# Optimization experiments

Hardware: AMD Instinct MI355X
Metric: run time of the kernel (lower is better)

## Reference

```python
import jax, jax.numpy as jnp
import numpy as np

B, S, Dm, H, W, G = 2, 4096, 768, 12, 256, 16
HD = Dm // H
NEG = -10000.0


def _band_qk(q, k, w):
    # q,k: [B,S,H,D] -> banded scores [B,S,H,2w+1]; slot j = key position i-w+j
    Bq, Sq, Hq, Dq = q.shape
    nb = Sq // w
    qb = q.reshape(Bq, nb, w, Hq, Dq)
    kp = jnp.pad(k, ((0, 0), (w, w), (0, 0), (0, 0)))
    idx = (jnp.arange(nb) * w)[:, None] + jnp.arange(3 * w)[None, :]
    kb = kp[:, idx]                                    # [B,nb,3w,H,D]
    s = jnp.einsum('btxhd,btyhd->bthxy', qb, kb)       # [B,nb,H,w,3w]
    r = jnp.arange(w)[:, None]
    c = r + jnp.arange(2 * w + 1)[None, :]
    band = s[..., r, c]                                # [B,nb,H,w,2w+1]
    return band.transpose(0, 1, 3, 2, 4).reshape(Bq, Sq, Hq, 2 * w + 1)


def _band_pv(p, v, w):
    # p: [B,S,H,2w+1], v: [B,S,H,D] -> [B,S,H,D]
    Bp, Sp, Hp, _ = p.shape
    Dv = v.shape[-1]
    nb = Sp // w
    vp = jnp.pad(v, ((0, 0), (w, w), (0, 0), (0, 0)))
    idx = (jnp.arange(nb) * w)[:, None] + jnp.arange(3 * w)[None, :]
    vb = vp[:, idx]                                    # [B,nb,3w,H,D]
    pb = p.reshape(Bp, nb, w, Hp, 2 * w + 1).transpose(0, 1, 3, 2, 4)
    r = jnp.arange(w)[:, None]
    c = r + jnp.arange(2 * w + 1)[None, :]
    pband = jnp.zeros((Bp, nb, Hp, w, 3 * w), p.dtype).at[..., r, c].set(pb)
    out = jnp.einsum('bthxy,btyhd->btxhd', pband, vb)  # [B,nb,w,H,D]
    return out.reshape(Bp, Sp, Hp, Dv)


def setup_inputs() -> dict:
    key = jax.random.key(0)
    ks = jax.random.split(key, 13)
    inp = {'hidden_states': jax.random.normal(ks[0], (B, S, Dm), dtype=jnp.float32)}
    names = ['Wq', 'bq', 'Wk', 'bk', 'Wv', 'bv', 'Wqg', 'bqg', 'Wkg', 'bkg', 'Wvg', 'bvg']
    for i, n in enumerate(names):
        sh = (Dm, Dm) if n.startswith('W') else (Dm,)
        inp[n] = 0.02 * jax.random.normal(ks[i + 1], sh, dtype=jnp.float32)
    inp['n_global'] = G
    return inp


def reference(hidden_states, Wq, bq, Wk, bk, Wv, bv, Wqg, bqg, Wkg, bkg, Wvg, bvg, n_global):
    Bh, Sh, D = hidden_states.shape
    hd = D // H
    w, g = W, n_global
    scale = 1.0 / jnp.sqrt(jnp.float32(hd))
    q = ((hidden_states @ Wq + bq) * scale).reshape(Bh, Sh, H, hd)
    k = (hidden_states @ Wk + bk).reshape(Bh, Sh, H, hd)
    v = (hidden_states @ Wv + bv).reshape(Bh, Sh, H, hd)
    # banded local attention scores (mask_invalid_locations -> -inf outside seq)
    band = _band_qk(q, k, w)                           # [B,S,H,2w+1]
    i = jnp.arange(Sh)[:, None]
    j = jnp.arange(2 * w + 1)[None, :]
    kpos = i - w + j                                   # key position per window slot
    valid = (kpos >= 0) & (kpos < Sh)
    band = jnp.where(valid[None, :, None, :], band, -jnp.inf)
    # remove global keys from windowed attention (-10000 float mask)
    band = band + jnp.where(valid & (kpos < g), NEG, 0.0)[None, :, None, :]
    # global columns: every query attends to global keys (local k projection)
    sel = jnp.einsum('bihd,bghd->bihg', q, k[:, :g])
    logits = jnp.concatenate([sel, band], axis=-1)     # [B,S,H,g+2w+1]
    probs = jax.nn.softmax(logits.astype(jnp.float32), axis=-1)
    attn = jnp.einsum('bihg,bghd->bihd', probs[..., :g], v[:, :g])
    attn = attn + _band_pv(probs[..., g:], v, w)       # [B,S,H,hd]
    # global token rows: full attention with global projections
    qg = ((hidden_states[:, :g] @ Wqg + bqg) * scale).reshape(Bh, g, H, hd)
    kg = (hidden_states @ Wkg + bkg).reshape(Bh, Sh, H, hd)
    vg = (hidden_states @ Wvg + bvg).reshape(Bh, Sh, H, hd)
    gl = jnp.einsum('bghd,bshd->bhgs', qg, kg)
    gp = jax.nn.softmax(gl.astype(jnp.float32), axis=-1)
    out_g = jnp.einsum('bhgs,bshd->bghd', gp, vg)      # [B,g,H,hd]
    attn = attn.at[:, :g].set(out_g)
    return attn.reshape(Bh, Sh, D)
```

## Files before the change

kernel.cpp:

```cpp
#include <hip/hip_runtime.h>

constexpr int Bc = 2, Sc = 4096, Dmc = 768, Hc = 12, HDc = 64, Wc = 256, Gc = 16;
constexpr int NCH = 16, CHK = 256;
constexpr float LOG2E = 1.4426950408889634f;
constexpr float SCALE2q = 0.125f * LOG2E;
constexpr float NEG2c = -10000.0f * LOG2E;

typedef __attribute__((ext_vector_type(8))) short s16x8;
typedef __attribute__((ext_vector_type(4))) short s16x4;
typedef __attribute__((ext_vector_type(4))) float f32x4;
typedef __attribute__((ext_vector_type(2))) unsigned int u32x2;

#define DEVINL __device__ __forceinline__

DEVINL float b2f(short x) {
  unsigned int u = ((unsigned int)(unsigned short)x) << 16;
  return __builtin_bit_cast(float, u);
}
DEVINL short f2b(float f) {
  unsigned int u = __builtin_bit_cast(unsigned int, f);
  unsigned int r = (u + 0x7fffu + ((u >> 16) & 1u)) >> 16;
  return (short)r;
}
DEVINL void gload16(const short* g, const short* l) {
  __builtin_amdgcn_global_load_lds(
      (const __attribute__((address_space(1))) void*)g,
      (__attribute__((address_space(3))) void*)l, 16, 0, 0);
}

__global__ __launch_bounds__(256) void conv_bf16(
    const float* __restrict__ src, short* __restrict__ dst)
{
  const size_t i = ((size_t)blockIdx.x * 256 + threadIdx.x) * 8;
  f32x4 a = *(const f32x4*)(src + i);
  f32x4 c = *(const f32x4*)(src + i + 4);
  s16x8 r;
#pragma unroll
  for (int u = 0; u < 4; ++u) { r[u] = f2b(a[u]); r[4 + u] = f2b(c[u]); }
  *(s16x8*)(dst + i) = r;
}

__global__ __launch_bounds__(256) void transpose_w(
    const float* __restrict__ W0, const float* __restrict__ W1, const float* __restrict__ W2,
    short* __restrict__ T0, short* __restrict__ T1, short* __restrict__ T2)
{
  const float* W = blockIdx.z == 0 ? W0 : (blockIdx.z == 1 ? W1 : W2);
  short* T = blockIdx.z == 0 ? T0 : (blockIdx.z == 1 ? T1 : T2);
  __shared__ short t[32][33];
  const int k0 = blockIdx.x * 32, n0 = blockIdx.y * 32;
  const int a = threadIdx.x >> 3, cg = (threadIdx.x & 7) * 4;
  f32x4 v = *(const f32x4*)&W[(size_t)(k0 + a) * Dmc + n0 + cg];
#pragma unroll
  for (int u = 0; u < 4; ++u) t[a][cg + u] = f2b(v[u]);
  __syncthreads();
  s16x4 s;
#pragma unroll
  for (int u = 0; u < 4; ++u) s[u] = t[cg + u][a];
  *(s16x4*)&T[(size_t)(n0 + a) * Dmc + k0 + cg] = s;
}

__global__ __launch_bounds__(256) void gemm_fused(
    const short* __restrict__ X, const short* __restrict__ Wt,
    const float* __restrict__ b0, const float* __restrict__ b1, const float* __restrict__ b2,
    short* __restrict__ Y0, float scale0)
{
  __shared__ short lds[16384];
  char* ldsb = (char*)lds;
  const int tid = threadIdx.x, lane = tid & 63, wid = tid >> 6;
  const int gy = gridDim.y;

  const int rawd = blockIdx.x + 64 * blockIdx.y;
  const int wgid = (rawd & 7) * (gy * 8) + (rawd >> 3);
  const int mi0 = wgid / gy, ny = wgid - mi0 * gy;
  const int m0 = mi0 * 128;
  const int nch = ny / 6, ncol = (ny % 6) * 128;
  const int n0g = ny * 128;

  short* Y = Y0 + (size_t)nch * 6291456;
  const float* bias = nch == 0 ? b0 : (nch == 1 ? b1 : b2);
  const float scale = nch == 0 ? scale0 : 1.0f;

  const int lr = lane & 15, lq = lane >> 4;
  const int wm = (wid & 1) * 64, wn = (wid >> 1) * 64;

  const int l8 = lane >> 3, l7 = lane & 7;
  const int colsh = ((l7 * 16) ^ (l8 << 4)) >> 1;
  const short* Aptr[4];
  const short* Bptr[4];
#pragma unroll
  for (int i = 0; i < 4; ++i) {
    Aptr[i] = X  + (size_t)(m0  + wid * 32 + i * 8 + l8) * Dmc + colsh;
    Bptr[i] = Wt + (size_t)(n0g + wid * 32 + i * 8 + l8) * Dmc + colsh;
  }

  int arb[4][2], brb[4][2];
#pragma unroll
  for (int mi = 0; mi < 4; ++mi)
#pragma unroll
    for (int ks = 0; ks < 2; ++ks) {
      int row = wm + mi * 16 + lr;
      arb[mi][ks] = row * 128 + ((lq * 16 + ks * 64) ^ ((row & 7) << 4));
    }
#pragma unroll
  for (int ni = 0; ni < 4; ++ni)
#pragma unroll
    for (int ks = 0; ks < 2; ++ks) {
      int row = wn + ni * 16 + lr;
      brb[ni][ks] = 16384 + row * 128 + ((lq * 16 + ks * 64) ^ ((row & 7) << 4));
    }

  f32x4 acc[4][4] = {};

  for (int kt = 0; kt < 12; ++kt) {
    const int ko = kt * 64;
    if (kt) __syncthreads();
#pragma unroll
    for (int i = 0; i < 4; ++i) {
      gload16(Aptr[i] + ko, &lds[wid * 2048 + i * 512]);
      gload16(Bptr[i] + ko, &lds[8192 + wid * 2048 + i * 512]);
    }
    asm volatile("s_waitcnt vmcnt(0)" ::: "memory");
    __syncthreads();
#pragma unroll
    for (int ks = 0; ks < 2; ++ks) {
      s16x8 af[4], bf[4];
#pragma unroll
      for (int mi = 0; mi < 4; ++mi) af[mi] = *(const s16x8*)(ldsb + arb[mi][ks]);
#pragma unroll
      for (int ni = 0; ni < 4; ++ni) bf[ni] = *(const s16x8*)(ldsb + brb[ni][ks]);
#pragma unroll
      for (int mi = 0; mi < 4; ++mi)
#pragma unroll
        for (int ni = 0; ni < 4; ++ni)
          acc[mi][ni] = __builtin_amdgcn_mfma_f32_16x16x32_bf16(af[mi], bf[ni], acc[mi][ni], 0, 0, 0);
    }
  }

#pragma unroll
  for (int mi = 0; mi < 4; ++mi)
#pragma unroll
    for (int ni = 0; ni < 4; ++ni) {
      int col = ncol + wn + ni * 16 + lr;
      float bv_ = bias[col];
#pragma unroll
      for (int r = 0; r < 4; ++r) {
        int row = m0 + wm + mi * 16 + lq * 4 + r;
        Y[(size_t)row * Dmc + col] = f2b((acc[mi][ni][r] + bv_) * scale);
      }
    }
}

__global__ __launch_bounds__(256) void qg_proj(
    const float* __restrict__ hs, const float* __restrict__ Wqg,
    const float* __restrict__ bqg, float* __restrict__ qg)
{
  const int row = blockIdx.x;
  const int b = row / Gc, i = row % Gc;
  const int tid = threadIdx.x;
  const int n = blockIdx.y * 128 + (tid & 127);
  const int half = tid >> 7;
  __shared__ float x[Dmc];
  __shared__ float part[128];
  for (int c = tid; c < Dmc; c += 256)
    x[c] = b2f(f2b(hs[((size_t)(b * Sc + i)) * Dmc + c]));
  __syncthreads();
  float acc = 0.f;
#pragma unroll 4
  for (int c = half * 384; c < half * 384 + 384; ++c)
    acc = fmaf(x[c], b2f(f2b(Wqg[(size_t)c * Dmc + n])), acc);
  if (half) part[tid & 127] = acc;
  __syncthreads();
  if (!half)
    qg[(size_t)row * Dmc + n] = (acc + part[tid] + bqg[n]) * SCALE2q;
}

__global__ __launch_bounds__(256) void local_attn_mfma(
    const short* __restrict__ q, const short* __restrict__ k,
    const short* __restrict__ v, float* __restrict__ out)
{
  const int raw = blockIdx.x + 64 * (blockIdx.y + 12 * blockIdx.z);
  const int swz = (raw & 7) * 192 + (raw >> 3);
  const int q0 = (swz & 63) * 64;
  const int h = (swz >> 6) % 12, b = swz / 768;
  const int tid = threadIdx.x, lane = tid & 63, wid = tid >> 6;

  __shared__ short Ks[4096];
  __shared__ short Vt[4096];
  __shared__ short Ps[4][1024];
  char* KsB = (char*)Ks;
  char* VtB = (char*)Vt;

  const int ql = lane & 15;
  const int lg = lane >> 4;
  const int qr = wid * 16 + ql;

  s16x8 qf[2];
  {
    const short* qp = q + ((size_t)(b * Sc + q0 + qr)) * Dmc + h * HDc + lg * 8;
    qf[0] = *(const s16x8*)qp;
    qf[1] = *(const s16x8*)(qp + 32);
  }

  f32x4 oacc[4] = {};
  float m_run = -INFINITY, l_run = 0.f;

  const int krow = tid >> 3, kcol16 = (tid & 7) * 16;
  const int vp = tid & 31, vo = tid >> 5;
  const size_t hoff = (size_t)h * HDc;
  const size_t brow = (size_t)b * Sc;

  auto keyof = [&](int c) {
    int key = (c < Gc) ? c : q0 - 272 + c;
    return min(max(key, 0), Sc - 1);
  };

  s16x8 kreg0, kreg1, vreg0, vreg1;
  auto loadRegs = [&](int ch) {
    kreg0 = *(const s16x8*)(k + (brow + keyof(ch * 64 + krow))      * Dmc + hoff + (kcol16 >> 1));
    kreg1 = *(const s16x8*)(k + (brow + keyof(ch * 64 + 32 + krow)) * Dmc + hoff + (kcol16 >> 1));
    vreg0 = *(const s16x8*)(v + (brow + keyof(ch * 64 + 2 * vp))     * Dmc + hoff + vo * 8);
    vreg1 = *(const s16x8*)(v + (brow + keyof(ch * 64 + 2 * vp + 1)) * Dmc + hoff + vo * 8);
  };

  loadRegs(0);

  for (int ch = 0; ch < 10; ++ch) {
    __syncthreads();
    *(s16x8*)(KsB + krow * 128        + (kcol16 ^ ((krow & 7) << 4))) = kreg0;
    *(s16x8*)(KsB + (krow + 32) * 128 + (kcol16 ^ ((krow & 7) << 4))) = kreg1;
#pragma unroll
    for (int j = 0; j < 8; ++j) {
      int d = vo * 8 + j;
      unsigned int wrd = (unsigned int)(unsigned short)vreg0[j] |
                         ((unsigned int)(unsigned short)vreg1[j] << 16);
      *(unsigned int*)(VtB + d * 128 + ((4 * vp) ^ (j << 4))) = wrd;
    }
    if (ch < 9) loadRegs(ch + 1);
    __syncthreads();

    f32x4 sac[4] = {};
    __builtin_amdgcn_s_setprio(1);
#pragma unroll
    for (int kt = 0; kt < 4; ++kt) {
      int row = kt * 16 + ql;
#pragma unroll
      for (int sl = 0; sl < 2; ++sl) {
        s16x8 af = *(const s16x8*)(KsB + row * 128 + ((lg * 16 + sl * 64) ^ ((row & 7) << 4)));
        sac[kt] = __builtin_amdgcn_mfma_f32_16x16x32_bf16(af, qf[sl], sac[kt], 0, 0, 0);
      }
    }
    __builtin_amdgcn_s_setprio(0);

    bool needMask = (ch < 2) | (ch > 7) | (q0 < 272) | (q0 > Sc - 384);
    if (needMask) {
#pragma unroll
      for (int kt = 0; kt < 4; ++kt)
#pragma unroll
        for (int r = 0; r < 4; ++r) {
          int c = ch * 64 + kt * 16 + lg * 4 + r;
          if (c >= Gc) {
            float sv = sac[kt][r];
            int jj = c - Gc - qr;
            int kp2 = q0 - 272 + c;
            bool ok = (jj >= 0) & (jj <= 2 * Wc) & (kp2 >= 0) & (kp2 < Sc);
            sac[kt][r] = ok ? (sv + ((kp2 < Gc) ? NEG2c : 0.f)) : -INFINITY;
          }
        }
    }

    float cm = -INFINITY;
#pragma unroll
    for (int kt = 0; kt < 4; ++kt)
#pragma unroll
      for (int r = 0; r < 4; ++r) cm = fmaxf(cm, sac[kt][r]);
    cm = fmaxf(cm, __shfl_xor(cm, 16));
    cm = fmaxf(cm, __shfl_xor(cm, 32));

    if (__all(cm <= m_run + 11.5f)) {
      float cl = 0.f;
#pragma unroll
      for (int kt = 0; kt < 4; ++kt)
#pragma unroll
        for (int r = 0; r < 4; ++r) {
          float p = exp2f(sac[kt][r] - m_run);
          sac[kt][r] = p;
          cl += p;
        }
      cl += __shfl_xor(cl, 16);
      cl += __shfl_xor(cl, 32);
      l_run += cl;
    } else {
      float m_new = fmaxf(m_run, cm);
      float scale = exp2f(m_run - m_new);
      float cl = 0.f;
#pragma unroll
      for (int kt = 0; kt < 4; ++kt)
#pragma unroll
        for (int r = 0; r < 4; ++r) {
          float p = exp2f(sac[kt][r] - m_new);
          sac[kt][r] = p;
          cl += p;
        }
      cl += __shfl_xor(cl, 16);
      cl += __shfl_xor(cl, 32);
      l_run = l_run * scale + cl;
      m_run = m_new;
#pragma unroll
      for (int rr = 0; rr < 4; ++rr) {
        float os = __shfl(scale, lg * 4 + rr);
#pragma unroll
        for (int dt = 0; dt < 4; ++dt) oacc[dt][rr] *= os;
      }
    }

    char* PsB = (char*)Ps[wid];
#pragma unroll
    for (int kt = 0; kt < 4; ++kt) {
      u32x2 pw;
      asm("v_cvt_pk_bf16_f32 %0, %1, %2" : "=v"(pw.x) : "v"(sac[kt][0]), "v"(sac[kt][1]));
      asm("v_cvt_pk_bf16_f32 %0, %1, %2" : "=v"(pw.y) : "v"(sac[kt][2]), "v"(sac[kt][3]));
      *(u32x2*)(PsB + ql * 128 + ((kt * 32 + lg * 8) ^ ((ql & 7) << 4))) = pw;
    }
    s16x8 pf[2];
#pragma unroll
    for (int ks = 0; ks < 2; ++ks)
      pf[ks] = *(const s16x8*)(PsB + ql * 128 + ((ks * 64 + lg * 16) ^ ((ql & 7) << 4)));
    __builtin_amdgcn_s_setprio(1);
#pragma unroll
    for (int dt = 0; dt < 4; ++dt) {
      int d = dt * 16 + ql;
#pragma unroll
      for (int ks = 0; ks < 2; ++ks) {
        s16x8 vf = *(const s16x8*)(VtB + d * 128 + ((ks * 64 + lg * 16) ^ ((d & 7) << 4)));
        oacc[dt] = __builtin_amdgcn_mfma_f32_16x16x32_bf16(pf[ks], vf, oacc[dt], 0, 0, 0);
      }
    }
    __builtin_amdgcn_s_setprio(0);
  }

  float inv = 1.f / l_run;
#pragma unroll
  for (int rr = 0; rr < 4; ++rr) {
    float oi = __shfl(inv, lg * 4 + rr);
    int row = q0 + wid * 16 + lg * 4 + rr;
    float* op = out + ((size_t)(b * Sc + row)) * Dmc + h * HDc + ql;
#pragma unroll
    for (int dt = 0; dt < 4; ++dt)
      op[dt * 16] = oacc[dt][rr] * oi;
  }
}

__global__ __launch_bounds__(256) void global_attn_part(
    const float* __restrict__ qg, const short* __restrict__ kg,
    const short* __restrict__ vg, float* __restrict__ pml, float* __restrict__ po)
{
  const int ch = blockIdx.x & (NCH - 1);
  const int i  = blockIdx.x >> 4;
  const int h = blockIdx.y, b = blockIdx.z;
  const int tid = threadIdx.x, lane = tid & 63, wid = tid >> 6;

  __shared__ float qrow[64];
  __shared__ float pls[CHK];
  __shared__ float red[8];
  __shared__ float osum[4][64];

  if (tid < 64) qrow[tid] = qg[(size_t)(b * Gc + i) * Dmc + h * HDc + tid];
  __syncthreads();

  const int sk = ch * CHK + tid;
  const s16x8* kr = (const s16x8*)(kg + ((size_t)(b * Sc + sk)) * Dmc + h * HDc);
  float acc = 0.f;
#pragma unroll
  for (int c = 0; c < 8; ++c) {
    s16x8 kv = kr[c];
#pragma unroll
    for (int u = 0; u < 8; ++u) acc = fmaf(qrow[c * 8 + u], b2f(kv[u]), acc);
  }

  float m = acc;
#pragma unroll
  for (int off = 32; off > 0; off >>= 1) m = fmaxf(m, __shfl_xor(m, off));
  if (lane == 0) red[wid] = m;
  __syncthreads();
  m = fmaxf(fmaxf(red[0], red[1]), fmaxf(red[2], red[3]));

  float p = exp2f(acc - m);
  pls[tid] = p;
  float ls = p;
#pragma unroll
  for (int off = 32; off > 0; off >>= 1) ls += __shfl_xor(ls, off);
  if (lane == 0) red[4 + wid] = ls;
  __syncthreads();
  const float l = red[4] + red[5] + red[6] + red[7];

  const int jg = tid >> 3, db = (tid & 7) * 8;
  float o[8] = {};
  const short* vb2 = vg + ((size_t)(b * Sc + ch * CHK + jg * 8)) * Dmc + h * HDc + db;
#pragma unroll
  for (int jj = 0; jj < 8; ++jj) {
    float pw = pls[jg * 8 + jj];
    s16x8 vv = *(const s16x8*)(vb2 + (size_t)jj * Dmc);
#pragma unroll
    for (int u = 0; u < 8; ++u) o[u] = fmaf(pw, b2f(vv[u]), o[u]);
  }
#pragma unroll
  for (int mk = 8; mk <= 32; mk <<= 1)
#pragma unroll
    for (int u = 0; u < 8; ++u) o[u] += __shfl_xor(o[u], mk);
  if ((lane & 56) == 0) {
#pragma unroll
    for (int u = 0; u < 8; ++u) osum[wid][(lane & 7) * 8 + u] = o[u];
  }
  __syncthreads();

  const size_t slot = (((size_t)(b * Hc + h) * Gc + i) * NCH + ch);
  if (tid < 64)
    po[slot * 64 + tid] = osum[0][tid] + osum[1][tid] + osum[2][tid] + osum[3][tid];
  if (tid == 0) { pml[slot * 2] = m; pml[slot * 2 + 1] = l; }
}

__global__ __launch_bounds__(64) void global_attn_comb(
    const float* __restrict__ pml, const float* __restrict__ po,
    float* __restrict__ out)
{
  const int i = blockIdx.x, h = blockIdx.y, b = blockIdx.z;
  const int d = threadIdx.x;
  const size_t base = ((size_t)(b * Hc + h) * Gc + i) * NCH;

  float m = -INFINITY;
#pragma unroll
  for (int ch = 0; ch < NCH; ++ch) m = fmaxf(m, pml[(base + ch) * 2]);
  float l = 0.f, o = 0.f;
#pragma unroll
  for (int ch = 0; ch < NCH; ++ch) {
    float wgt = exp2f(pml[(base + ch) * 2] - m);
    l = fmaf(pml[(base + ch) * 2 + 1], wgt, l);
    o = fmaf(po[(base + ch) * 64 + d], wgt, o);
  }
  out[((size_t)(b * Sc + i)) * Dmc + h * HDc + d] = o / l;
}

extern "C" void kernel_launch(void* const* d_in, const int* in_sizes, int n_in,
                              void* d_out, int out_size, void* d_ws, size_t ws_size,
                              hipStream_t stream) {
  const float* hs  = (const float*)d_in[0];
  const float* Wq  = (const float*)d_in[1];
  const float* bq  = (const float*)d_in[2];
  const float* Wk  = (const float*)d_in[3];
  const float* bk  = (const float*)d_in[4];
  const float* Wv  = (const float*)d_in[5];
  const float* bv  = (const float*)d_in[6];
  const float* Wqg = (const float*)d_in[7];
  const float* bqg = (const float*)d_in[8];
  const float* Wkg = (const float*)d_in[9];
  const float* bkg = (const float*)d_in[10];
  const float* Wvg = (const float*)d_in[11];
  const float* bvg = (const float*)d_in[12];
  float* out = (float*)d_out;

  char* ws = (char*)d_ws;
  const size_t bufB = (size_t)Bc * Sc * Dmc * sizeof(short);
  short* hsb = (short*)(ws);
  short* s1  = (short*)(ws + bufB);
  short* s2  = (short*)(ws + 2 * bufB);
  short* s3  = (short*)(ws + 3 * bufB);

  short* wtA = (short*)d_out;
  short* wtB = wtA + (size_t)Dmc * Dmc;
  short* wtC = wtB + (size_t)Dmc * Dmc;
  float* qg  = (float*)(ws + 3 * bufB);
  float* pml = (float*)(ws + 3 * bufB + 98304);
  float* po  = (float*)(ws + 3 * bufB + 147456);
  short* wtD = (short*)(ws + 3 * bufB + (4u << 20));
  short* wtE = wtD + (size_t)Dmc * Dmc;

  dim3 bb(256);
  conv_bf16<<<dim3(3072), bb, 0, stream>>>(hs, hsb);
  transpose_w<<<dim3(24, 24, 3), bb, 0, stream>>>(Wq, Wk, Wv, wtA, wtB, wtC);

  gemm_fused<<<dim3(64, 18), bb, 0, stream>>>(hsb, wtA, bq, bk, bv, s1, SCALE2q);

  local_attn_mfma<<<dim3(64, Hc, Bc), bb, 0, stream>>>(s1, s2, s3, out);

  transpose_w<<<dim3(24, 24, 2), bb, 0, stream>>>(Wkg, Wvg, Wvg, wtD, wtE, wtE);
  gemm_fused<<<dim3(64, 12), bb, 0, stream>>>(hsb, wtD, bkg, bvg, bvg, s1, 1.0f);

  qg_proj<<<dim3(Bc * Gc, Dmc / 128), bb, 0, stream>>>(hs, Wqg, bqg, qg);
  global_attn_part<<<dim3(Gc * NCH, Hc, Bc), bb, 0, stream>>>(qg, s1, s2, pml, po);
  global_attn_comb<<<dim3(Gc, Hc, Bc), dim3(64), 0, stream>>>(pml, po, out);
}
```

Measured before the change: 194.2 us.

## Skip masked last chunk for most waves, use raw exp2, incremental pointers, max3 reduction

Several micro-optimizations land in the windowed attention kernel. In chunk 9 only wave 3 does the QK/softmax/PV work, because the other waves' query rows see only masked keys there. Interior blocks advance their K/V load pointers by a fixed stride instead of recomputing clamped key indices. The row max uses a three-input max tree, exp2f is replaced by the hardware __builtin_amdgcn_exp2f with four partial sums, and the global kernels also switch to the raw exp2. The raw exp2 skips denormal/range handling, and the wave skip relies on the band geometry being exact.

Result: faster. 189.5 us (-2.4%).

```diff
diff --git a/kernel.cpp b/kernel.cpp
--- a/kernel.cpp
+++ b/kernel.cpp
@@ -27,6 +27,7 @@
       (const __attribute__((address_space(1))) void*)g,
       (__attribute__((address_space(3))) void*)l, 16, 0, 0);
 }
+DEVINL float max3f(float a, float b, float c) { return fmaxf(fmaxf(a, b), c); }
 
 __global__ __launch_bounds__(256) void conv_bf16(
     const float* __restrict__ src, short* __restrict__ dst)
@@ -209,17 +210,28 @@
   const size_t hoff = (size_t)h * HDc;
   const size_t brow = (size_t)b * Sc;
 
+  const bool interior = (q0 >= 256) && (q0 <= Sc - 384);
+
   auto keyof = [&](int c) {
     int key = (c < Gc) ? c : q0 - 272 + c;
     return min(max(key, 0), Sc - 1);
   };
 
+  const short *kp0, *kp1, *vp0, *vp1;
   s16x8 kreg0, kreg1, vreg0, vreg1;
   auto loadRegs = [&](int ch) {
-    kreg0 = *(const s16x8*)(k + (brow + keyof(ch * 64 + krow))      * Dmc + hoff + (kcol16 >> 1));
-    kreg1 = *(const s16x8*)(k + (brow + keyof(ch * 64 + 32 + krow)) * Dmc + hoff + (kcol16 >> 1));
-    vreg0 = *(const s16x8*)(v + (brow + keyof(ch * 64 + 2 * vp))     * Dmc + hoff + vo * 8);
-    vreg1 = *(const s16x8*)(v + (brow + keyof(ch * 64 + 2 * vp + 1)) * Dmc + hoff + vo * 8);
+    if (!interior || ch <= 1) {
+      kp0 = k + (brow + keyof(ch * 64 + krow))       * Dmc + hoff + (kcol16 >> 1);
+      kp1 = k + (brow + keyof(ch * 64 + 32 + krow))  * Dmc + hoff + (kcol16 >> 1);
+      vp0 = v + (brow + keyof(ch * 64 + 2 * vp))      * Dmc + hoff + vo * 8;
+      vp1 = v + (brow + keyof(ch * 64 + 2 * vp + 1))  * Dmc + hoff + vo * 8;
+    } else {
+      kp0 += 64 * Dmc; kp1 += 64 * Dmc; vp0 += 64 * Dmc; vp1 += 64 * Dmc;
+    }
+    kreg0 = *(const s16x8*)kp0;
+    kreg1 = *(const s16x8*)kp1;
+    vreg0 = *(const s16x8*)vp0;
+    vreg1 = *(const s16x8*)vp1;
   };
 
   loadRegs(0);
@@ -237,6 +249,8 @@
     }
     if (ch < 9) loadRegs(ch + 1);
     __syncthreads();
+
+    if (ch == 9 && wid != 3) continue;
 
     f32x4 sac[4] = {};
     __builtin_amdgcn_s_setprio(1);
@@ -268,39 +282,44 @@
         }
     }
 
-    float cm = -INFINITY;
-#pragma unroll
-    for (int kt = 0; kt < 4; ++kt)
-#pragma unroll
-      for (int r = 0; r < 4; ++r) cm = fmaxf(cm, sac[kt][r]);
+    float t0 = max3f(sac[0][0], sac[0][1], sac[0][2]);
+    float t1 = max3f(sac[0][3], sac[1][0], sac[1][1]);
+    float t2 = max3f(sac[1][2], sac[1][3], sac[2][0]);
+    float t3 = max3f(sac[2][1], sac[2][2], sac[2][3]);
+    float t4 = max3f(sac[3][0], sac[3][1], sac[3][2]);
+    float cm = fmaxf(max3f(t0, t1, t2), max3f(t3, t4, sac[3][3]));
     cm = fmaxf(cm, __shfl_xor(cm, 16));
     cm = fmaxf(cm, __shfl_xor(cm, 32));
 
     if (__all(cm <= m_run + 11.5f)) {
-      float cl = 0.f;
-#pragma unroll
-      for (int kt = 0; kt < 4; ++kt)
-#pragma unroll
-        for (int r = 0; r < 4; ++r) {
-          float p = exp2f(sac[kt][r] - m_run);
-          sac[kt][r] = p;
-          cl += p;
-        }
+      float cl0 = 0.f, cl1 = 0.f, cl2 = 0.f, cl3 = 0.f;
+#pragma unroll
+      for (int kt = 0; kt < 4; ++kt) {
+        float p0 = __builtin_amdgcn_exp2f(sac[kt][0] - m_run);
+        float p1 = __builtin_amdgcn_exp2f(sac[kt][1] - m_run);
+        float p2 = __builtin_amdgcn_exp2f(sac[kt][2] - m_run);
+        float p3 = __builtin_amdgcn_exp2f(sac[kt][3] - m_run);
+        sac[kt][0] = p0; sac[kt][1] = p1; sac[kt][2] = p2; sac[kt][3] = p3;
+        cl0 += p0; cl1 += p1; cl2 += p2; cl3 += p3;
+      }
+      float cl = (cl0 + cl1) + (cl2 + cl3);
       cl += __shfl_xor(cl, 16);
       cl += __shfl_xor(cl, 32);
       l_run += cl;
     } else {
       float m_new = fmaxf(m_run, cm);
-      float scale = exp2f(m_run - m_new);
-      float cl = 0.f;
-#pragma unroll
-      for (int kt = 0; kt < 4; ++kt)
-#pragma unroll
-        for (int r = 0; r < 4; ++r) {
-          float p = exp2f(sac[kt][r] - m_new);
-          sac[kt][r] = p;
-          cl += p;
-        }
+      float scale = __builtin_amdgcn_exp2f(m_run - m_new);
+      float cl0 = 0.f, cl1 = 0.f, cl2 = 0.f, cl3 = 0.f;
+#pragma unroll
+      for (int kt = 0; kt < 4; ++kt) {
+        float p0 = __builtin_amdgcn_exp2f(sac[kt][0] - m_new);
+        float p1 = __builtin_amdgcn_exp2f(sac[kt][1] - m_new);
+        float p2 = __builtin_amdgcn_exp2f(sac[kt][2] - m_new);
+        float p3 = __builtin_amdgcn_exp2f(sac[kt][3] - m_new);
+        sac[kt][0] = p0; sac[kt][1] = p1; sac[kt][2] = p2; sac[kt][3] = p3;
+        cl0 += p0; cl1 += p1; cl2 += p2; cl3 += p3;
+      }
+      float cl = (cl0 + cl1) + (cl2 + cl3);
       cl += __shfl_xor(cl, 16);
       cl += __shfl_xor(cl, 32);
       l_run = l_run * scale + cl;
@@ -384,7 +403,7 @@
   __syncthreads();
   m = fmaxf(fmaxf(red[0], red[1]), fmaxf(red[2], red[3]));
 
-  float p = exp2f(acc - m);
+  float p = __builtin_amdgcn_exp2f(acc - m);
   pls[tid] = p;
   float ls = p;
 #pragma unroll
@@ -433,7 +452,7 @@
   float l = 0.f, o = 0.f;
 #pragma unroll
   for (int ch = 0; ch < NCH; ++ch) {
-    float wgt = exp2f(pml[(base + ch) * 2] - m);
+    float wgt = __builtin_amdgcn_exp2f(pml[(base + ch) * 2] - m);
     l = fmaf(pml[(base + ch) * 2 + 1], wgt, l);
     o = fmaf(po[(base + ch) * 64 + d], wgt, o);
   }
```
